# Performance work log

Hardware: AMD Instinct MI355X
Metric: run time of the kernel (lower is better)

## Reference

```python
import jax, jax.numpy as jnp
import numpy as np

EPS = 1e-6
SLIDING_WINDOW = 512
ROPE_BASE = 10000.0  # rope_local_base_freq for sliding_attention layers


def _rms_norm(x, w=None):
    # Gemma-style RMSNorm computed in fp32 then cast back
    xf = x.astype(jnp.float32)
    out = xf * jax.lax.rsqrt(jnp.mean(xf * xf, axis=-1, keepdims=True) + EPS)
    if w is not None:
        out = out * w.astype(jnp.float32)
    return out.astype(x.dtype)


def _rotate_half(x):
    x1, x2 = jnp.split(x, 2, axis=-1)
    return jnp.concatenate((-x2, x1), axis=-1)


def setup_inputs() -> dict:
    key = jax.random.key(0)
    ks = jax.random.split(key, 6)
    B, S, H, NH, NKV, D = 1, 4096, 2048, 8, 2, 256
    hidden_states = jax.random.normal(ks[0], (B, S, H), dtype=jnp.float32)
    w_q = jax.random.normal(ks[1], (H, NH * D), dtype=jnp.float32) * 0.02
    w_k = jax.random.normal(ks[2], (H, NKV * D), dtype=jnp.float32) * 0.02
    w_v = jax.random.normal(ks[3], (H, NKV * D), dtype=jnp.float32) * 0.02
    w_o = jax.random.normal(ks[4], (NH * D, H), dtype=jnp.float32) * 0.02
    q_norm_w = jnp.ones((D,), dtype=jnp.float32)
    k_norm_w = jnp.ones((D,), dtype=jnp.float32)
    # RoPE tables (local base freq, sliding layer)
    inv_freq = 1.0 / (ROPE_BASE ** (jnp.arange(0, D, 2, dtype=jnp.float32) / D))
    pos = jnp.arange(S, dtype=jnp.float32)
    freqs = pos[:, None] * inv_freq[None, :]          # [S, D/2]
    emb = jnp.concatenate((freqs, freqs), axis=-1)    # [S, D]
    cos = jnp.broadcast_to(jnp.cos(emb)[None], (B, S, D)).astype(jnp.float32)
    sin = jnp.broadcast_to(jnp.sin(emb)[None], (B, S, D)).astype(jnp.float32)
    return {"hidden_states": hidden_states, "w_q": w_q, "w_k": w_k, "w_v": w_v,
            "w_o": w_o, "q_norm_w": q_norm_w, "k_norm_w": k_norm_w,
            "cos": cos, "sin": sin}


def reference(hidden_states, w_q, w_k, w_v, w_o, q_norm_w, k_norm_w, cos, sin):
    B, S, _ = hidden_states.shape
    D = cos.shape[-1]
    NH = w_q.shape[1] // D
    NKV = w_k.shape[1] // D
    G = NH // NKV

    # projections -> [B, S, heads, D], per-head RMSNorm (Gemma3n-style)
    q = _rms_norm((hidden_states @ w_q).reshape(B, S, NH, D), q_norm_w)
    k = _rms_norm((hidden_states @ w_k).reshape(B, S, NKV, D), k_norm_w)
    v = _rms_norm((hidden_states @ w_v).reshape(B, S, NKV, D))  # v_norm: no scale

    q = q.transpose(0, 2, 1, 3)  # [B, NH, S, D]
    k = k.transpose(0, 2, 1, 3)  # [B, NKV, S, D]
    v = v.transpose(0, 2, 1, 3)

    # RoPE, cos/sin unsqueezed over the head dim
    c = cos[:, None, :, :]
    s = sin[:, None, :, :]
    q = q * c + _rotate_half(q) * s
    k = k * c + _rotate_half(k) * s

    # GQA: repeat KV heads
    k = jnp.repeat(k, G, axis=1)  # [B, NH, S, D]
    v = jnp.repeat(v, G, axis=1)

    # attention, scaling = 1.0 (q_norm replaces 1/sqrt(d) in this family)
    scores = jnp.einsum('bhqd,bhkd->bhqk', q, k)

    # causal + sliding-window mask
    i = jnp.arange(S)[:, None]
    j = jnp.arange(S)[None, :]
    mask = (j <= i) & ((i - j) < SLIDING_WINDOW)
    scores = jnp.where(mask[None, None], scores, jnp.finfo(scores.dtype).min)

    attn = jax.nn.softmax(scores.astype(jnp.float32), axis=-1).astype(q.dtype)
    out = jnp.einsum('bhqk,bhkd->bhqd', attn, v)
    out = out.transpose(0, 2, 1, 3).reshape(B, S, NH * D)
    return out @ w_o
```

## Files before the change

### kernel.cpp

```cpp
#include <hip/hip_runtime.h>
#include <hip/hip_bf16.h>

#define S_LEN 4096
#define HDIM  2048
#define NHQ   8
#define NKVH  2
#define DHEAD 256
#define WIN   512
#define NQKV  3072

typedef __hip_bfloat16 bf16_t;
using fragAB = __attribute__((ext_vector_type(8))) short;
using fragC  = __attribute__((ext_vector_type(4))) float;

typedef unsigned int u32;
typedef const __attribute__((address_space(1))) u32* gas_ptr;
typedef __attribute__((address_space(3))) u32* las_ptr;

__device__ __forceinline__ void async_copy16(const void* g, void* l) {
  __builtin_amdgcn_global_load_lds((gas_ptr)g, (las_ptr)l, 16, 0, 0);
}

#define NEG_BIG (-3.0e38f)

__device__ __forceinline__ void split2(float x, bf16_t& hi, bf16_t& lo) {
  bf16_t h = __float2bfloat16(x);
  hi = h;
  lo = __float2bfloat16(x - (float)h);
}

__global__ __launch_bounds__(256) void split_f32(
    const float* __restrict__ in, bf16_t* __restrict__ hi,
    bf16_t* __restrict__ lo, int n) {
  int i = (blockIdx.x * 256 + threadIdx.x) * 4;
  if (i >= n) return;
  float4 v = *(const float4*)(in + i);
  split2(v.x, hi[i + 0], lo[i + 0]);
  split2(v.y, hi[i + 1], lo[i + 1]);
  split2(v.z, hi[i + 2], lo[i + 2]);
  split2(v.w, hi[i + 3], lo[i + 3]);
}

__global__ __launch_bounds__(256) void transpose_cvt(
    const float* __restrict__ in, bf16_t* __restrict__ out, int R, int C) {
  __shared__ bf16_t tile[32][33];
  int c0 = blockIdx.x * 32, r0 = blockIdx.y * 32;
  int tx = threadIdx.x & 31, ty = threadIdx.x >> 5;
#pragma unroll
  for (int i = 0; i < 4; ++i)
    tile[ty + i * 8][tx] = __float2bfloat16(in[(size_t)(r0 + ty + i * 8) * C + c0 + tx]);
  __syncthreads();
#pragma unroll
  for (int i = 0; i < 4; ++i)
    out[(size_t)(c0 + ty + i * 8) * R + r0 + tx] = tile[tx][ty + i * 8];
}

__global__ __launch_bounds__(256) void transpose_split_fused(
    const float* __restrict__ wq, const float* __restrict__ wk,
    const float* __restrict__ wv, bf16_t* __restrict__ hiT,
    bf16_t* __restrict__ loT) {
  __shared__ bf16_t th[32][33];
  __shared__ bf16_t tl[32][33];
  int oc = blockIdx.x * 32;
  int r0 = blockIdx.y * 32;
  const float* src; int C, c0;
  if (oc < 2048)      { src = wq; C = 2048; c0 = oc; }
  else if (oc < 2560) { src = wk; C = 512;  c0 = oc - 2048; }
  else                { src = wv; C = 512;  c0 = oc - 2560; }
  int tx = threadIdx.x & 31, ty = threadIdx.x >> 5;
#pragma unroll
  for (int i = 0; i < 4; ++i) {
    float x = src[(size_t)(r0 + ty + i * 8) * C + c0 + tx];
    bf16_t h, l; split2(x, h, l);
    th[ty + i * 8][tx] = h;
    tl[ty + i * 8][tx] = l;
  }
  __syncthreads();
#pragma unroll
  for (int i = 0; i < 4; ++i) {
    hiT[(size_t)(oc + ty + i * 8) * HDIM + r0 + tx] = th[tx][ty + i * 8];
    loT[(size_t)(oc + ty + i * 8) * HDIM + r0 + tx] = tl[tx][ty + i * 8];
  }
}

#define VMCNT_(n) asm volatile("s_waitcnt vmcnt(" #n ")" ::: "memory")
#define VMCNT(n) VMCNT_(n)
#define BARRIER()                     \
  {                                   \
    asm volatile("" ::: "memory");    \
    __builtin_amdgcn_s_barrier();     \
    asm volatile("" ::: "memory");    \
  }

#define MFMA_(a, b, c) __builtin_amdgcn_mfma_f32_16x16x32_bf16(a, b, c, 0, 0, 0)

#define OFF_AH 0
#define OFF_AL 16384
#define OFF_BH 32768
#define OFF_BL 45056
#define BUFSZ  57344

#define LOADB()                                                   \
  _Pragma("unroll")                                               \
  for (int j = 0; j < 3; ++j) {                                   \
    const char* bp_ = bufc + (wn + j * 16 + l16) * 64 + rdq;      \
    bh[j] = *(const fragAB*)(bp_ + OFF_BH);                       \
    bl[j] = *(const fragAB*)(bp_ + OFF_BL);                       \
  }

struct ARegs { fragAB ah0, al0, ah1, al1; };

__device__ __forceinline__ void lda_split(ARegs& r, const char* bufc, int wm,
                                          int p, int l16, int rdq) {
  const char* a0 = bufc + (wm + (2 * p) * 16 + l16) * 64 + rdq;
  const char* a1 = a0 + 16 * 64;
  r.ah0 = *(const fragAB*)(a0 + OFF_AH);
  r.al0 = *(const fragAB*)(a0 + OFF_AL);
  r.ah1 = *(const fragAB*)(a1 + OFF_AH);
  r.al1 = *(const fragAB*)(a1 + OFF_AL);
}

__device__ __forceinline__ void mfma_split(fragC (&acc)[8][3], const ARegs& r,
                                           const fragAB (&bh)[3],
                                           const fragAB (&bl)[3], int p) {
  __builtin_amdgcn_s_setprio(1);
#pragma unroll
  for (int j = 0; j < 3; ++j) {
    acc[2 * p][j]     = MFMA_(r.al0, bh[j], acc[2 * p][j]);
    acc[2 * p + 1][j] = MFMA_(r.al1, bh[j], acc[2 * p + 1][j]);
  }
#pragma unroll
  for (int j = 0; j < 3; ++j) {
    acc[2 * p][j]     = MFMA_(r.ah0, bl[j], acc[2 * p][j]);
    acc[2 * p + 1][j] = MFMA_(r.ah1, bl[j], acc[2 * p + 1][j]);
  }
#pragma unroll
  for (int j = 0; j < 3; ++j) {
    acc[2 * p][j]     = MFMA_(r.ah0, bh[j], acc[2 * p][j]);
    acc[2 * p + 1][j] = MFMA_(r.ah1, bh[j], acc[2 * p + 1][j]);
  }
  __builtin_amdgcn_s_setprio(0);
}

#define SPLIT_STEP()                        \
  {                                         \
    LOADB();                                \
    lda_split(r0, bufc, wm, 0, l16, rdq);   \
    lda_split(r1, bufc, wm, 1, l16, rdq);   \
    mfma_split(acc, r0, bh, bl, 0);         \
    lda_split(r0, bufc, wm, 2, l16, rdq);   \
    mfma_split(acc, r1, bh, bl, 1);         \
    lda_split(r1, bufc, wm, 3, l16, rdq);   \
    mfma_split(acc, r0, bh, bl, 2);         \
    mfma_split(acc, r1, bh, bl, 3);         \
  }

__global__ __launch_bounds__(512, 2) void gemm_split2(
    const bf16_t* __restrict__ Ah, const bf16_t* __restrict__ Al,
    const bf16_t* __restrict__ Bh, const bf16_t* __restrict__ Bl,
    float* __restrict__ C, int M, int N, int K) {
  __shared__ __align__(16) char lds[2 * BUFSZ];
  const int t = threadIdx.x;
  const int wave = t >> 6, lane = t & 63;
  const int quad = lane >> 4, l16 = lane & 15;
  const int g = blockIdx.y * 16 + blockIdx.x;
  const int lby = (g & 7) * 2 + ((g >> 3) >> 4);
  const int lbx = (g >> 3) & 15;
  const int m0 = lby * 256, n0 = lbx * 192;
  const int wm = (wave >> 2) * 128, wn = (wave & 3) * 48;
  const int rdq = (quad ^ ((l16 >> 1) & 3)) * 16;

  const size_t laneOff =
      (size_t)(lane >> 2) * K * 2 + 16 * ((lane & 3) ^ ((lane >> 3) & 3));

  const char* gsrc[7];
  int ldsOff[7];
#pragma unroll
  for (int pos = 0; pos < 3; ++pos) {
    int c = wave + 8 * pos;
    if (c < 12) {
      gsrc[pos]   = (const char*)Bh + (size_t)(n0 + 16 * c) * K * 2 + laneOff;
      ldsOff[pos] = OFF_BH + c * 1024;
    } else {
      gsrc[pos]   = (const char*)Bl + (size_t)(n0 + 16 * (c - 12)) * K * 2 + laneOff;
      ldsOff[pos] = OFF_BL + (c - 12) * 1024;
    }
  }
#pragma unroll
  for (int p = 0; p < 4; ++p) {
    int sub = wave & 3;
    int R0 = ((sub >> 1) & 1) * 128 + 32 * p + (sub & 1) * 16;
    const char* base = (const char*)(wave < 4 ? Ah : Al);
    gsrc[3 + p]   = base + (size_t)(m0 + R0) * K * 2 + laneOff;
    ldsOff[3 + p] = (wave < 4 ? OFF_AH : OFF_AL) + R0 * 64;
  }

  fragC zero4 = {0.f, 0.f, 0.f, 0.f};
  fragC acc[8][3];
#pragma unroll
  for (int i = 0; i < 8; ++i)
#pragma unroll
    for (int j = 0; j < 3; ++j) acc[i][j] = zero4;

  char* ldsc = (char*)lds;
#pragma unroll
  for (int ps = 0; ps < 7; ++ps) async_copy16(gsrc[ps], ldsc + ldsOff[ps]);
#pragma unroll
  for (int ps = 0; ps < 7; ++ps) gsrc[ps] += 64;

  fragAB bh[3], bl[3];
  ARegs r0, r1;
  int cur = 0;
  const int NS = K / 32;
  for (int it = 0; it < NS - 1; ++it) {
    const char* bufc = ldsc + cur * BUFSZ;
    char* nb = ldsc + (cur ^ 1) * BUFSZ;
    VMCNT(0); BARRIER();
#pragma unroll
    for (int ps = 0; ps < 7; ++ps) async_copy16(gsrc[ps], nb + ldsOff[ps]);
#pragma unroll
    for (int ps = 0; ps < 7; ++ps) gsrc[ps] += 64;
    SPLIT_STEP();
    cur ^= 1;
  }
  {
    const char* bufc = ldsc + cur * BUFSZ;
    VMCNT(0); BARRIER();
    SPLIT_STEP();
  }

#pragma unroll
  for (int i = 0; i < 8; ++i)
#pragma unroll
    for (int j = 0; j < 3; ++j)
#pragma unroll
      for (int r = 0; r < 4; ++r) {
        int row = m0 + wm + i * 16 + quad * 4 + r;
        int col = n0 + wn + j * 16 + l16;
        C[(size_t)row * N + col] = acc[i][j][r];
      }
}

#define BT_OFF_A 0
#define BT_OFF_B 32768
#define BT_BUFSZ 49152

struct ARegs2 { fragAB a[2][2]; };

__device__ __forceinline__ void lda_bt(ARegs2& r, const char* bufc, int wm,
                                       int p, int l16, int quad, int rx) {
#pragma unroll
  for (int u = 0; u < 2; ++u)
#pragma unroll
    for (int ks = 0; ks < 2; ++ks)
      r.a[u][ks] = *(const fragAB*)(bufc + BT_OFF_A +
                                    (wm + (2 * p + u) * 16 + l16) * 128 +
                                    (((ks * 4 + quad) ^ rx) * 16));
}

__device__ __forceinline__ void mfma_bt(fragC (&acc)[8][2], const ARegs2& r,
                                        const fragAB (&b)[2][2], int p) {
  __builtin_amdgcn_s_setprio(1);
#pragma unroll
  for (int ks = 0; ks < 2; ++ks)
#pragma unroll
    for (int j = 0; j < 2; ++j) {
      acc[2 * p][j]     = MFMA_(r.a[0][ks], b[j][ks], acc[2 * p][j]);
      acc[2 * p + 1][j] = MFMA_(r.a[1][ks], b[j][ks], acc[2 * p + 1][j]);
    }
  __builtin_amdgcn_s_setprio(0);
}

#define BT_LOADB()                                                        \
  _Pragma("unroll")                                                       \
  for (int j = 0; j < 2; ++j)                                             \
  _Pragma("unroll")                                                       \
    for (int ks = 0; ks < 2; ++ks)                                        \
      bfr[j][ks] = *(const fragAB*)(bufc + BT_OFF_B +                     \
                                    (wn + j * 16 + l16) * 128 +           \
                                    (((ks * 4 + quad) ^ rx) * 16));

#define BT_STEP()                                 \
  {                                               \
    BT_LOADB();                                   \
    lda_bt(r0, bufc, wm, 0, l16, quad, rx);       \
    lda_bt(r1, bufc, wm, 1, l16, quad, rx);       \
    mfma_bt(acc, r0, bfr, 0);                     \
    lda_bt(r0, bufc, wm, 2, l16, quad, rx);       \
    mfma_bt(acc, r1, bfr, 1);                     \
    lda_bt(r1, bufc, wm, 3, l16, quad, rx);       \
    mfma_bt(acc, r0, bfr, 2);                     \
    mfma_bt(acc, r1, bfr, 3);                     \
  }

__global__ __launch_bounds__(512, 2) void gemm_bt2(
    const bf16_t* __restrict__ A, const bf16_t* __restrict__ Bt,
    float* __restrict__ C, int M, int N, int K) {
  __shared__ __align__(16) char lds[2 * BT_BUFSZ];
  const int t = threadIdx.x;
  const int wave = t >> 6, lane = t & 63;
  const int quad = lane >> 4, l16 = lane & 15;
  const int g = blockIdx.y * 16 + blockIdx.x;
  const int lby = (g & 7) * 2 + ((g >> 3) >> 4);
  const int lbx = (g >> 3) & 15;
  const int m0 = lby * 256, n0 = lbx * 128;
  const int wm = (wave >> 2) * 128, wn = (wave & 3) * 32;
  const int rx = l16 & 7;

  const size_t laneOff =
      (size_t)(lane >> 3) * K * 2 + 16 * ((lane & 7) ^ ((lane >> 3) & 7));

  const char* gsrc[6];
  int ldsOff[6];
#pragma unroll
  for (int pos = 0; pos < 2; ++pos) {
    int c = wave + 8 * pos;
    gsrc[pos]   = (const char*)Bt + (size_t)(n0 + 8 * c) * K * 2 + laneOff;
    ldsOff[pos] = BT_OFF_B + c * 1024;
  }
#pragma unroll
  for (int p = 0; p < 4; ++p) {
    int R0 = (wave >> 2) * 128 + 32 * p + (wave & 3) * 8;
    gsrc[2 + p]   = (const char*)A + (size_t)(m0 + R0) * K * 2 + laneOff;
    ldsOff[2 + p] = BT_OFF_A + R0 * 128;
  }

  fragC zero4 = {0.f, 0.f, 0.f, 0.f};
  fragC acc[8][2];
#pragma unroll
  for (int i = 0; i < 8; ++i)
#pragma unroll
    for (int j = 0; j < 2; ++j) acc[i][j] = zero4;

  char* ldsc = (char*)lds;
#pragma unroll
  for (int ps = 0; ps < 6; ++ps) async_copy16(gsrc[ps], ldsc + ldsOff[ps]);
#pragma unroll
  for (int ps = 0; ps < 6; ++ps) gsrc[ps] += 128;

  fragAB bfr[2][2];
  ARegs2 r0, r1;
  int cur = 0;
  const int NS = K / 64;
  for (int it = 0; it < NS - 1; ++it) {
    const char* bufc = ldsc + cur * BT_BUFSZ;
    char* nb = ldsc + (cur ^ 1) * BT_BUFSZ;
    VMCNT(0); BARRIER();
#pragma unroll
    for (int ps = 0; ps < 6; ++ps) async_copy16(gsrc[ps], nb + ldsOff[ps]);
#pragma unroll
    for (int ps = 0; ps < 6; ++ps) gsrc[ps] += 128;
    BT_STEP();
    cur ^= 1;
  }
  {
    const char* bufc = ldsc + cur * BT_BUFSZ;
    VMCNT(0); BARRIER();
    BT_STEP();
  }

#pragma unroll
  for (int i = 0; i < 8; ++i)
#pragma unroll
    for (int j = 0; j < 2; ++j)
#pragma unroll
      for (int r = 0; r < 4; ++r) {
        int row = m0 + wm + i * 16 + quad * 4 + r;
        int col = n0 + wn + j * 16 + l16;
        C[(size_t)row * N + col] = acc[i][j][r];
      }
}

__global__ __launch_bounds__(256) void rmsnorm_rope_split_qk(
    const float* __restrict__ proj, const float* __restrict__ qnw,
    const float* __restrict__ knw, const float* __restrict__ cosb,
    const float* __restrict__ sinb, bf16_t* __restrict__ qhi,
    bf16_t* __restrict__ qlo, bf16_t* __restrict__ khi,
    bf16_t* __restrict__ klo) {
  int s = blockIdx.x, hb = blockIdx.y, d = threadIdx.x;
  const float* w; bf16_t* oh; bf16_t* ol; int inOff, outStride, oBase;
  if (hb < NHQ) {
    w = qnw; oh = qhi; ol = qlo;
    inOff = hb * DHEAD; outStride = NHQ * DHEAD; oBase = hb * DHEAD;
  } else {
    int hk = hb - NHQ;
    w = knw; oh = khi; ol = klo;
    inOff = NHQ * DHEAD + hk * DHEAD; outStride = NKVH * DHEAD; oBase = hk * DHEAD;
  }
  float x = proj[(size_t)s * NQKV + inOff + d];
  float ss = x * x;
  ss += __shfl_xor(ss, 1);  ss += __shfl_xor(ss, 2);  ss += __shfl_xor(ss, 4);
  ss += __shfl_xor(ss, 8);  ss += __shfl_xor(ss, 16); ss += __shfl_xor(ss, 32);
  __shared__ float part[4];
  __shared__ float xs[DHEAD];
  if ((threadIdx.x & 63) == 0) part[threadIdx.x >> 6] = ss;
  __syncthreads();
  float tot = part[0] + part[1] + part[2] + part[3];
  float r = rsqrtf(tot * (1.0f / DHEAD) + 1e-6f);
  float xn = x * r * w[d];
  xs[d] = xn;
  __syncthreads();
  float other = xs[(d + 128) & 255];
  float rot = (d < 128) ? -other : other;
  float y = xn * cosb[(size_t)s * DHEAD + d] + rot * sinb[(size_t)s * DHEAD + d];
  bf16_t h2, l2; split2(y, h2, l2);
  size_t oidx = (size_t)s * outStride + oBase + d;
  oh[oidx] = h2;
  ol[oidx] = l2;
}

__global__ __launch_bounds__(256) void rmsnorm_vT2(
    const float* __restrict__ proj, bf16_t* __restrict__ vt, int inOff) {
  __shared__ float rs_[32];
  __shared__ bf16_t tile[32][33];
  int s0 = blockIdx.x * 32, hh = blockIdx.y;
  const float* base = proj + (size_t)s0 * NQKV + inOff + hh * DHEAD;
  int t = threadIdx.x;
  int sl = t >> 3, c8 = t & 7;
  const float4* rowp = (const float4*)(base + (size_t)sl * NQKV + c8 * 32);
  float ss = 0.f;
#pragma unroll
  for (int i = 0; i < 8; ++i) {
    float4 v = rowp[i];
    ss += v.x * v.x + v.y * v.y + v.z * v.z + v.w * v.w;
  }
  ss += __shfl_xor(ss, 1); ss += __shfl_xor(ss, 2); ss += __shfl_xor(ss, 4);
  if (c8 == 0) rs_[sl] = rsqrtf(ss * (1.0f / DHEAD) + 1e-6f);
  __syncthreads();
  int tx = t & 31, ty = t >> 5;
#pragma unroll
  for (int ch = 0; ch < 8; ++ch) {
#pragma unroll
    for (int i = 0; i < 4; ++i) {
      int s_ = ty + i * 8;
      float x = base[(size_t)s_ * NQKV + ch * 32 + tx];
      tile[s_][tx] = __float2bfloat16(x * rs_[s_]);
    }
    __syncthreads();
#pragma unroll
    for (int i = 0; i < 4; ++i) {
      int dl = ty + i * 8;
      vt[((size_t)hh * DHEAD + ch * 32 + dl) * S_LEN + s0 + tx] = tile[tx][dl];
    }
    __syncthreads();
  }
}

__global__ __launch_bounds__(512, 2) void attn_split(
    const bf16_t* __restrict__ Qhi, const bf16_t* __restrict__ Qlo,
    const bf16_t* __restrict__ Khi, const bf16_t* __restrict__ Klo,
    const bf16_t* __restrict__ Vt, bf16_t* __restrict__ Aout) {
  const int g = blockIdx.y * 32 + blockIdx.x;
  const int lbx = (g & 7) * 4 + ((g >> 3) & 3);
  const int h = g >> 5;
  const int qb = lbx * 128;
  const int wave = threadIdx.x >> 6, lane = threadIdx.x & 63;
  const int quad = lane >> 4, l16 = lane & 15;
  const int qw = qb + wave * 16;
  const int kv = h >> 2;
  const bf16_t* Qh_ = Qhi + h * DHEAD;
  const bf16_t* Ql_ = Qlo + h * DHEAD;
  const bf16_t* Kh_ = Khi + kv * DHEAD;
  const bf16_t* Kl_ = Klo + kv * DHEAD;
  const bf16_t* Vh_ = Vt + (size_t)kv * DHEAD * S_LEN;

  __shared__ __align__(16) bf16_t KshH[2][32 * 256];
  __shared__ __align__(16) bf16_t KshL[2][32 * 256];
  __shared__ __align__(16) bf16_t Vsh[2][256 * 32];
  __shared__ __align__(16) bf16_t Plds[8][16 * 32];

  fragAB qfh[8], qfl[8];
#pragma unroll
  for (int c = 0; c < 8; ++c) {
    size_t off = (size_t)(qw + l16) * (NHQ * DHEAD) + c * 32 + quad * 8;
    qfh[c] = *(const fragAB*)(Qh_ + off);
    qfl[c] = *(const fragAB*)(Ql_ + off);
  }

  int kRow[2], kCol[2], vRow[2], vCol[2];
#pragma unroll
  for (int i = 0; i < 2; ++i) {
    int ci = i * 512 + threadIdx.x;
    kRow[i] = ci >> 5;
    kCol[i] = ((ci & 31) ^ (kRow[i] & 31)) * 8;
    vRow[i] = ci >> 2;
    vCol[i] = ((ci & 3) ^ (vRow[i] & 3)) * 8;
  }

#define ASTAGE(buf, kb_)                                                     \
  _Pragma("unroll")                                                          \
  for (int i = 0; i < 2; ++i) {                                              \
    size_t dst = (size_t)(i * 512 + threadIdx.x) * 16;                       \
    size_t koff = (size_t)((kb_) + kRow[i]) * (NKVH * DHEAD) + kCol[i];      \
    async_copy16(Kh_ + koff, (char*)KshH[buf] + dst);                        \
    async_copy16(Kl_ + koff, (char*)KshL[buf] + dst);                        \
    async_copy16(Vh_ + (size_t)vRow[i] * S_LEN + (kb_) + vCol[i],            \
                 (char*)Vsh[buf] + dst);                                     \
  }

  fragC zero4 = {0.f, 0.f, 0.f, 0.f};
  fragC o_acc[16];
#pragma unroll
  for (int c = 0; c < 16; ++c) o_acc[c] = zero4;
  float m_run[4] = {NEG_BIG, NEG_BIG, NEG_BIG, NEG_BIG};
  float l_run[4] = {0.f, 0.f, 0.f, 0.f};
  const float LOG2E = 1.4426950408889634f;

  int k_lo = qb - (WIN - 1);
  if (k_lo < 0) k_lo = 0;
  k_lo &= ~31;

  ASTAGE(0, k_lo);
  int cur = 0;

  for (int kb = k_lo; kb < qb + 128; kb += 32) {
    VMCNT(0); BARRIER();
    if (kb + 32 < qb + 128) {
      int nbuf = cur ^ 1;
      ASTAGE(nbuf, kb + 32);
    }
    const char* KH = (const char*)KshH[cur];
    const char* KL = (const char*)KshL[cur];
    const char* VB = (const char*)Vsh[cur];

    fragC s[2] = {zero4, zero4};
    __builtin_amdgcn_s_setprio(1);
#pragma unroll
    for (int c = 0; c < 8; ++c) {
      int j = c * 4 + quad;
#pragma unroll
      for (int gg = 0; gg < 2; ++gg) {
        int row = gg * 16 + l16;
        int off = (row * 32 + (j ^ (row & 31))) * 16;
        fragAB kh = *(const fragAB*)(KH + off);
        fragAB kl = *(const fragAB*)(KL + off);
        s[gg] = __builtin_amdgcn_mfma_f32_16x16x32_bf16(qfl[c], kh, s[gg], 0, 0, 0);
        s[gg] = __builtin_amdgcn_mfma_f32_16x16x32_bf16(qfh[c], kl, s[gg], 0, 0, 0);
        s[gg] = __builtin_amdgcn_mfma_f32_16x16x32_bf16(qfh[c], kh, s[gg], 0, 0, 0);
      }
    }
    __builtin_amdgcn_s_setprio(0);

    float p[2][4], alpha[4];
#pragma unroll
    for (int r = 0; r < 4; ++r) {
      int qi = qw + quad * 4 + r;
      bool vld[2];
      float mx = NEG_BIG;
#pragma unroll
      for (int gg = 0; gg < 2; ++gg) {
        int ki = kb + gg * 16 + l16;
        vld[gg] = (ki <= qi) && (qi - ki < WIN);
        mx = fmaxf(mx, vld[gg] ? s[gg][r] : NEG_BIG);
      }
      mx = fmaxf(mx, __shfl_xor(mx, 1));
      mx = fmaxf(mx, __shfl_xor(mx, 2));
      mx = fmaxf(mx, __shfl_xor(mx, 4));
      mx = fmaxf(mx, __shfl_xor(mx, 8));
      float mn = fmaxf(m_run[r], mx);
      float a  = exp2f(fmaxf(m_run[r] - mn, -80.f) * LOG2E);
      float rs = 0.f;
#pragma unroll
      for (int gg = 0; gg < 2; ++gg) {
        float e = vld[gg] ? exp2f(fmaxf(s[gg][r] - mn, -80.f) * LOG2E) : 0.f;
        p[gg][r] = e;
        rs += e;
      }
      rs += __shfl_xor(rs, 1);
      rs += __shfl_xor(rs, 2);
      rs += __shfl_xor(rs, 4);
      rs += __shfl_xor(rs, 8);
      l_run[r] = l_run[r] * a + rs;
      m_run[r] = mn;
      alpha[r] = a;
    }
#pragma unroll
    for (int c = 0; c < 16; ++c)
#pragma unroll
      for (int r = 0; r < 4; ++r) o_acc[c][r] *= alpha[r];

    bf16_t* Pw = Plds[wave];
#pragma unroll
    for (int r = 0; r < 4; ++r)
#pragma unroll
      for (int gg = 0; gg < 2; ++gg)
        Pw[(quad * 4 + r) * 32 + gg * 16 + l16] = __float2bfloat16(p[gg][r]);
    fragAB pf = *(const fragAB*)((const char*)Pw + l16 * 64 + quad * 16);

    __builtin_amdgcn_s_setprio(1);
#pragma unroll
    for (int c = 0; c < 16; ++c) {
      int d = c * 16 + l16;
      int offv = (d * 4 + (quad ^ (d & 3))) * 16;
      fragAB vf = *(const fragAB*)(VB + offv);
      o_acc[c] = __builtin_amdgcn_mfma_f32_16x16x32_bf16(pf, vf, o_acc[c], 0, 0, 0);
    }
    __builtin_amdgcn_s_setprio(0);
    cur ^= 1;
  }

  float inv_l[4];
#pragma unroll
  for (int r = 0; r < 4; ++r) inv_l[r] = 1.0f / l_run[r];
#pragma unroll
  for (int c = 0; c < 16; ++c)
#pragma unroll
    for (int r = 0; r < 4; ++r) {
      int row = qw + quad * 4 + r;
      int col = h * DHEAD + c * 16 + l16;
      Aout[(size_t)row * (NHQ * DHEAD) + col] = __float2bfloat16(o_acc[c][r] * inv_l[r]);
    }
#undef ASTAGE
}

extern "C" void kernel_launch(void* const* d_in, const int* in_sizes, int n_in,
                              void* d_out, int out_size, void* d_ws, size_t ws_size,
                              hipStream_t stream) {
  const float* hid  = (const float*)d_in[0];
  const float* w_q  = (const float*)d_in[1];
  const float* w_k  = (const float*)d_in[2];
  const float* w_v  = (const float*)d_in[3];
  const float* w_o  = (const float*)d_in[4];
  const float* qnw  = (const float*)d_in[5];
  const float* knw  = (const float*)d_in[6];
  const float* cosb = (const float*)d_in[7];
  const float* sinb = (const float*)d_in[8];
  float* outp = (float*)d_out;

  const size_t M1 = 1048576;
  bf16_t* w = (bf16_t*)d_ws;
  bf16_t* hidh  = w;
  bf16_t* qh    = w;
  bf16_t* hidl  = w + 8 * M1;
  bf16_t* ql    = w + 8 * M1;
  bf16_t* wTh   = w + 16 * M1;
  bf16_t* kh    = w + 16 * M1;
  bf16_t* kl    = w + 18 * M1;
  bf16_t* vt    = w + 20 * M1;
  bf16_t* wTl   = w + 22 * M1;
  bf16_t* woT   = w + 22 * M1;
  float*  projqkv = (float*)(w + 28 * M1);
  bf16_t* aout  = w + 28 * M1;

  split_f32<<<(S_LEN * HDIM) / 1024, 256, 0, stream>>>(hid, hidh, hidl, S_LEN * HDIM);
  transpose_split_fused<<<dim3(NQKV / 32, HDIM / 32), 256, 0, stream>>>(
      w_q, w_k, w_v, wTh, wTl);

  gemm_split2<<<dim3(NQKV / 192, S_LEN / 256), 512, 0, stream>>>(
      hidh, hidl, wTh, wTl, projqkv, S_LEN, NQKV, HDIM);

  rmsnorm_rope_split_qk<<<dim3(S_LEN, NHQ + NKVH), 256, 0, stream>>>(
      projqkv, qnw, knw, cosb, sinb, qh, ql, kh, kl);
  rmsnorm_vT2<<<dim3(S_LEN / 32, NKVH), 256, 0, stream>>>(
      projqkv, vt, NHQ * DHEAD + NKVH * DHEAD);
  transpose_cvt<<<dim3(HDIM / 32, (NHQ * DHEAD) / 32), 256, 0, stream>>>(
      w_o, woT, NHQ * DHEAD, HDIM);

  attn_split<<<dim3(S_LEN / 128, NHQ), 512, 0, stream>>>(qh, ql, kh, kl, vt, aout);

  gemm_bt2<<<dim3(HDIM / 128, S_LEN / 256), 512, 0, stream>>>(
      aout, woT, outp, S_LEN, HDIM, NHQ * DHEAD);
}
```

Measured before the change: 404.0 us.

## Retile QKV split GEMM to 12 waves, vectorize split and RMSNorm-RoPE kernels

```diff
diff --git a/kernel.cpp b/kernel.cpp
--- a/kernel.cpp
+++ b/kernel.cpp
@@ -13,6 +13,9 @@
 using fragAB = __attribute__((ext_vector_type(8))) short;
 using fragC  = __attribute__((ext_vector_type(4))) float;
 
+struct __align__(8)  bf16x4 { bf16_t v[4]; };
+struct __align__(16) bf16x8 { bf16_t v[8]; };
+
 typedef unsigned int u32;
 typedef const __attribute__((address_space(1))) u32* gas_ptr;
 typedef __attribute__((address_space(3))) u32* las_ptr;
@@ -32,13 +35,16 @@
 __global__ __launch_bounds__(256) void split_f32(
     const float* __restrict__ in, bf16_t* __restrict__ hi,
     bf16_t* __restrict__ lo, int n) {
-  int i = (blockIdx.x * 256 + threadIdx.x) * 4;
+  int i = (blockIdx.x * 256 + threadIdx.x) * 8;
   if (i >= n) return;
-  float4 v = *(const float4*)(in + i);
-  split2(v.x, hi[i + 0], lo[i + 0]);
-  split2(v.y, hi[i + 1], lo[i + 1]);
-  split2(v.z, hi[i + 2], lo[i + 2]);
-  split2(v.w, hi[i + 3], lo[i + 3]);
+  float4 a = *(const float4*)(in + i);
+  float4 b = *(const float4*)(in + i + 4);
+  float xs[8] = {a.x, a.y, a.z, a.w, b.x, b.y, b.z, b.w};
+  bf16x8 hv, lv;
+#pragma unroll
+  for (int j = 0; j < 8; ++j) split2(xs[j], hv.v[j], lv.v[j]);
+  *(bf16x8*)(hi + i) = hv;
+  *(bf16x8*)(lo + i) = lv;
 }
 
 __global__ __launch_bounds__(256) void transpose_cvt(
@@ -100,62 +106,36 @@
 #define OFF_BL 45056
 #define BUFSZ  57344
 
-#define LOADB()                                                   \
-  _Pragma("unroll")                                               \
-  for (int j = 0; j < 3; ++j) {                                   \
-    const char* bp_ = bufc + (wn + j * 16 + l16) * 64 + rdq;      \
-    bh[j] = *(const fragAB*)(bp_ + OFF_BH);                       \
-    bl[j] = *(const fragAB*)(bp_ + OFF_BL);                       \
-  }
-
-struct ARegs { fragAB ah0, al0, ah1, al1; };
-
-__device__ __forceinline__ void lda_split(ARegs& r, const char* bufc, int wm,
-                                          int p, int l16, int rdq) {
-  const char* a0 = bufc + (wm + (2 * p) * 16 + l16) * 64 + rdq;
-  const char* a1 = a0 + 16 * 64;
-  r.ah0 = *(const fragAB*)(a0 + OFF_AH);
-  r.al0 = *(const fragAB*)(a0 + OFF_AL);
-  r.ah1 = *(const fragAB*)(a1 + OFF_AH);
-  r.al1 = *(const fragAB*)(a1 + OFF_AL);
-}
-
-__device__ __forceinline__ void mfma_split(fragC (&acc)[8][3], const ARegs& r,
-                                           const fragAB (&bh)[3],
-                                           const fragAB (&bl)[3], int p) {
-  __builtin_amdgcn_s_setprio(1);
-#pragma unroll
-  for (int j = 0; j < 3; ++j) {
-    acc[2 * p][j]     = MFMA_(r.al0, bh[j], acc[2 * p][j]);
-    acc[2 * p + 1][j] = MFMA_(r.al1, bh[j], acc[2 * p + 1][j]);
-  }
-#pragma unroll
-  for (int j = 0; j < 3; ++j) {
-    acc[2 * p][j]     = MFMA_(r.ah0, bl[j], acc[2 * p][j]);
-    acc[2 * p + 1][j] = MFMA_(r.ah1, bl[j], acc[2 * p + 1][j]);
-  }
-#pragma unroll
-  for (int j = 0; j < 3; ++j) {
-    acc[2 * p][j]     = MFMA_(r.ah0, bh[j], acc[2 * p][j]);
-    acc[2 * p + 1][j] = MFMA_(r.ah1, bh[j], acc[2 * p + 1][j]);
-  }
-  __builtin_amdgcn_s_setprio(0);
-}
-
-#define SPLIT_STEP()                        \
-  {                                         \
-    LOADB();                                \
-    lda_split(r0, bufc, wm, 0, l16, rdq);   \
-    lda_split(r1, bufc, wm, 1, l16, rdq);   \
-    mfma_split(acc, r0, bh, bl, 0);         \
-    lda_split(r0, bufc, wm, 2, l16, rdq);   \
-    mfma_split(acc, r1, bh, bl, 1);         \
-    lda_split(r1, bufc, wm, 3, l16, rdq);   \
-    mfma_split(acc, r0, bh, bl, 2);         \
-    mfma_split(acc, r1, bh, bl, 3);         \
-  }
-
-__global__ __launch_bounds__(512, 2) void gemm_split2(
+#define SPLIT_STEP()                                                    \
+  {                                                                     \
+    fragAB bh[4], bl[4];                                                \
+    _Pragma("unroll") for (int j = 0; j < 4; ++j) {                     \
+      const char* bp = bufc + (wn + j * 16 + l16) * 64 + rdq;           \
+      bh[j] = *(const fragAB*)(bp + OFF_BH);                            \
+      bl[j] = *(const fragAB*)(bp + OFF_BL);                            \
+    }                                                                   \
+    _Pragma("unroll") for (int p = 0; p < 2; ++p) {                     \
+      fragAB ah[2], al[2];                                              \
+      _Pragma("unroll") for (int u = 0; u < 2; ++u) {                   \
+        const char* ap = bufc + (wm + (2 * p + u) * 16 + l16) * 64 + rdq;\
+        ah[u] = *(const fragAB*)(ap + OFF_AH);                          \
+        al[u] = *(const fragAB*)(ap + OFF_AL);                          \
+      }                                                                 \
+      __builtin_amdgcn_s_setprio(1);                                    \
+      _Pragma("unroll") for (int j = 0; j < 4; ++j)                     \
+        _Pragma("unroll") for (int u = 0; u < 2; ++u)                   \
+          acc[2 * p + u][j] = MFMA_(al[u], bh[j], acc[2 * p + u][j]);   \
+      _Pragma("unroll") for (int j = 0; j < 4; ++j)                     \
+        _Pragma("unroll") for (int u = 0; u < 2; ++u)                   \
+          acc[2 * p + u][j] = MFMA_(ah[u], bl[j], acc[2 * p + u][j]);   \
+      _Pragma("unroll") for (int j = 0; j < 4; ++j)                     \
+        _Pragma("unroll") for (int u = 0; u < 2; ++u)                   \
+          acc[2 * p + u][j] = MFMA_(ah[u], bh[j], acc[2 * p + u][j]);   \
+      __builtin_amdgcn_s_setprio(0);                                    \
+    }                                                                   \
+  }
+
+__global__ __launch_bounds__(768, 3) void gemm_split2(
     const bf16_t* __restrict__ Ah, const bf16_t* __restrict__ Al,
     const bf16_t* __restrict__ Bh, const bf16_t* __restrict__ Bl,
     float* __restrict__ C, int M, int N, int K) {
@@ -167,59 +147,63 @@
   const int lby = (g & 7) * 2 + ((g >> 3) >> 4);
   const int lbx = (g >> 3) & 15;
   const int m0 = lby * 256, n0 = lbx * 192;
-  const int wm = (wave >> 2) * 128, wn = (wave & 3) * 48;
+  const int wm = (wave / 3) * 64, wn = (wave % 3) * 64;
   const int rdq = (quad ^ ((l16 >> 1) & 3)) * 16;
 
   const size_t laneOff =
       (size_t)(lane >> 2) * K * 2 + 16 * ((lane & 3) ^ ((lane >> 3) & 3));
 
-  const char* gsrc[7];
+  const char* gbase[7];
   int ldsOff[7];
-#pragma unroll
-  for (int pos = 0; pos < 3; ++pos) {
-    int c = wave + 8 * pos;
-    if (c < 12) {
-      gsrc[pos]   = (const char*)Bh + (size_t)(n0 + 16 * c) * K * 2 + laneOff;
-      ldsOff[pos] = OFF_BH + c * 1024;
-    } else {
-      gsrc[pos]   = (const char*)Bl + (size_t)(n0 + 16 * (c - 12)) * K * 2 + laneOff;
-      ldsOff[pos] = OFF_BL + (c - 12) * 1024;
-    }
-  }
-#pragma unroll
-  for (int p = 0; p < 4; ++p) {
-    int sub = wave & 3;
-    int R0 = ((sub >> 1) & 1) * 128 + 32 * p + (sub & 1) * 16;
-    const char* base = (const char*)(wave < 4 ? Ah : Al);
-    gsrc[3 + p]   = base + (size_t)(m0 + R0) * K * 2 + laneOff;
-    ldsOff[3 + p] = (wave < 4 ? OFF_AH : OFF_AL) + R0 * 64;
+  if (wave < 8) {
+#pragma unroll
+    for (int pos = 0; pos < 3; ++pos) {
+      int c = wave + 8 * pos;
+      if (c < 12) {
+        gbase[pos]  = (const char*)Bh + (size_t)(n0 + 16 * c) * K * 2;
+        ldsOff[pos] = OFF_BH + c * 1024;
+      } else {
+        gbase[pos]  = (const char*)Bl + (size_t)(n0 + 16 * (c - 12)) * K * 2;
+        ldsOff[pos] = OFF_BL + (c - 12) * 1024;
+      }
+    }
+#pragma unroll
+    for (int p = 0; p < 4; ++p) {
+      int sub = wave & 3;
+      int R0 = ((sub >> 1) & 1) * 128 + 32 * p + (sub & 1) * 16;
+      const char* base = (const char*)(wave < 4 ? Ah : Al);
+      gbase[3 + p]  = base + (size_t)(m0 + R0) * K * 2;
+      ldsOff[3 + p] = (wave < 4 ? OFF_AH : OFF_AL) + R0 * 64;
+    }
   }
 
   fragC zero4 = {0.f, 0.f, 0.f, 0.f};
-  fragC acc[8][3];
-#pragma unroll
-  for (int i = 0; i < 8; ++i)
-#pragma unroll
-    for (int j = 0; j < 3; ++j) acc[i][j] = zero4;
+  fragC acc[4][4];
+#pragma unroll
+  for (int i = 0; i < 4; ++i)
+#pragma unroll
+    for (int j = 0; j < 4; ++j) acc[i][j] = zero4;
 
   char* ldsc = (char*)lds;
-#pragma unroll
-  for (int ps = 0; ps < 7; ++ps) async_copy16(gsrc[ps], ldsc + ldsOff[ps]);
-#pragma unroll
-  for (int ps = 0; ps < 7; ++ps) gsrc[ps] += 64;
-
-  fragAB bh[3], bl[3];
-  ARegs r0, r1;
+  if (wave < 8) {
+#pragma unroll
+    for (int ps = 0; ps < 7; ++ps)
+      async_copy16(gbase[ps] + laneOff, ldsc + ldsOff[ps]);
+  }
+
+  size_t kk = 64;
   int cur = 0;
   const int NS = K / 32;
   for (int it = 0; it < NS - 1; ++it) {
     const char* bufc = ldsc + cur * BUFSZ;
     char* nb = ldsc + (cur ^ 1) * BUFSZ;
     VMCNT(0); BARRIER();
-#pragma unroll
-    for (int ps = 0; ps < 7; ++ps) async_copy16(gsrc[ps], nb + ldsOff[ps]);
-#pragma unroll
-    for (int ps = 0; ps < 7; ++ps) gsrc[ps] += 64;
+    if (wave < 8) {
+#pragma unroll
+      for (int ps = 0; ps < 7; ++ps)
+        async_copy16(gbase[ps] + kk + laneOff, nb + ldsOff[ps]);
+    }
+    kk += 64;
     SPLIT_STEP();
     cur ^= 1;
   }
@@ -230,9 +214,9 @@
   }
 
 #pragma unroll
-  for (int i = 0; i < 8; ++i)
-#pragma unroll
-    for (int j = 0; j < 3; ++j)
+  for (int i = 0; i < 4; ++i)
+#pragma unroll
+    for (int j = 0; j < 4; ++j)
 #pragma unroll
       for (int r = 0; r < 4; ++r) {
         int row = m0 + wm + i * 16 + quad * 4 + r;
@@ -371,13 +355,15 @@
       }
 }
 
-__global__ __launch_bounds__(256) void rmsnorm_rope_split_qk(
+__global__ __launch_bounds__(256) void rmsnorm_rope_qk2(
     const float* __restrict__ proj, const float* __restrict__ qnw,
     const float* __restrict__ knw, const float* __restrict__ cosb,
     const float* __restrict__ sinb, bf16_t* __restrict__ qhi,
     bf16_t* __restrict__ qlo, bf16_t* __restrict__ khi,
     bf16_t* __restrict__ klo) {
-  int s = blockIdx.x, hb = blockIdx.y, d = threadIdx.x;
+  const int wv = threadIdx.x >> 6, lane = threadIdx.x & 63;
+  const int idx = blockIdx.x * 4 + wv;
+  const int s = idx / (NHQ + NKVH), hb = idx % (NHQ + NKVH);
   const float* w; bf16_t* oh; bf16_t* ol; int inOff, outStride, oBase;
   if (hb < NHQ) {
     w = qnw; oh = qhi; ol = qlo;
@@ -387,26 +373,31 @@
     w = knw; oh = khi; ol = klo;
     inOff = NHQ * DHEAD + hk * DHEAD; outStride = NKVH * DHEAD; oBase = hk * DHEAD;
   }
-  float x = proj[(size_t)s * NQKV + inOff + d];
-  float ss = x * x;
+  const int d = lane * 4;
+  float4 x = *(const float4*)(proj + (size_t)s * NQKV + inOff + d);
+  float ss = x.x * x.x + x.y * x.y + x.z * x.z + x.w * x.w;
   ss += __shfl_xor(ss, 1);  ss += __shfl_xor(ss, 2);  ss += __shfl_xor(ss, 4);
   ss += __shfl_xor(ss, 8);  ss += __shfl_xor(ss, 16); ss += __shfl_xor(ss, 32);
-  __shared__ float part[4];
-  __shared__ float xs[DHEAD];
-  if ((threadIdx.x & 63) == 0) part[threadIdx.x >> 6] = ss;
-  __syncthreads();
-  float tot = part[0] + part[1] + part[2] + part[3];
-  float r = rsqrtf(tot * (1.0f / DHEAD) + 1e-6f);
-  float xn = x * r * w[d];
-  xs[d] = xn;
-  __syncthreads();
-  float other = xs[(d + 128) & 255];
-  float rot = (d < 128) ? -other : other;
-  float y = xn * cosb[(size_t)s * DHEAD + d] + rot * sinb[(size_t)s * DHEAD + d];
-  bf16_t h2, l2; split2(y, h2, l2);
-  size_t oidx = (size_t)s * outStride + oBase + d;
-  oh[oidx] = h2;
-  ol[oidx] = l2;
+  float r = rsqrtf(ss * (1.0f / DHEAD) + 1e-6f);
+  float4 w4 = *(const float4*)(w + d);
+  float xn[4] = {x.x * r * w4.x, x.y * r * w4.y, x.z * r * w4.z, x.w * r * w4.w};
+  float ot[4];
+#pragma unroll
+  for (int j = 0; j < 4; ++j) ot[j] = __shfl_xor(xn[j], 32);
+  float sgn = (lane < 32) ? -1.0f : 1.0f;
+  float4 c4 = *(const float4*)(cosb + (size_t)s * DHEAD + d);
+  float4 s4 = *(const float4*)(sinb + (size_t)s * DHEAD + d);
+  float cc[4] = {c4.x, c4.y, c4.z, c4.w};
+  float sn[4] = {s4.x, s4.y, s4.z, s4.w};
+  bf16x4 hv, lv;
+#pragma unroll
+  for (int j = 0; j < 4; ++j) {
+    float y = xn[j] * cc[j] + sgn * ot[j] * sn[j];
+    split2(y, hv.v[j], lv.v[j]);
+  }
+  size_t o = (size_t)s * outStride + oBase + d;
+  *(bf16x4*)(oh + o) = hv;
+  *(bf16x4*)(ol + o) = lv;
 }
 
 __global__ __launch_bounds__(256) void rmsnorm_vT2(
@@ -642,14 +633,14 @@
   float*  projqkv = (float*)(w + 28 * M1);
   bf16_t* aout  = w + 28 * M1;
 
-  split_f32<<<(S_LEN * HDIM) / 1024, 256, 0, stream>>>(hid, hidh, hidl, S_LEN * HDIM);
+  split_f32<<<(S_LEN * HDIM) / 2048, 256, 0, stream>>>(hid, hidh, hidl, S_LEN * HDIM);
   transpose_split_fused<<<dim3(NQKV / 32, HDIM / 32), 256, 0, stream>>>(
       w_q, w_k, w_v, wTh, wTl);
 
-  gemm_split2<<<dim3(NQKV / 192, S_LEN / 256), 512, 0, stream>>>(
+  gemm_split2<<<dim3(NQKV / 192, S_LEN / 256), 768, 0, stream>>>(
       hidh, hidl, wTh, wTl, projqkv, S_LEN, NQKV, HDIM);
 
-  rmsnorm_rope_split_qk<<<dim3(S_LEN, NHQ + NKVH), 256, 0, stream>>>(
+  rmsnorm_rope_qk2<<<(S_LEN * (NHQ + NKVH)) / 4, 256, 0, stream>>>(
       projqkv, qnw, knw, cosb, sinb, qh, ql, kh, kl);
   rmsnorm_vT2<<<dim3(S_LEN / 32, NKVH), 256, 0, stream>>>(
       projqkv, vt, NHQ * DHEAD + NKVH * DHEAD);
```

Measured after the change: 399.3 us. No clear change (-1.2%).
